# Kernel tuning notes

Hardware: AMD Instinct MI355X
Metric: run time of the kernel (lower is better)

## Reference

```python
import jax, jax.numpy as jnp
import numpy as np
import math

HEADS = 16
LN_EPS = 1e-5


def activation_quant(x):
    # 8-bit activation quant with straight-through estimator
    scale = 127.0 / jnp.clip(jnp.max(jnp.abs(x), axis=-1, keepdims=True), 1e-5)
    y = jnp.clip(jnp.round(x * scale), -128.0, 127.0) / scale
    return x + jax.lax.stop_gradient(y - x)


def weight_quant(w):
    # ternary {-1,0,1} weight quant with STE
    scale = 1.0 / jnp.clip(jnp.mean(jnp.abs(w)), 1e-5)
    wq = jnp.clip(jnp.round(w * scale), -1.0, 1.0) / scale
    return w + jax.lax.stop_gradient(wq - w)


def bitlinear(x, w):
    # F.layer_norm(x, x.shape[1:]) -> normalize jointly over (N, D), no affine
    mu = jnp.mean(x, axis=(1, 2), keepdims=True)
    var = jnp.var(x, axis=(1, 2), keepdims=True)
    xn = (x - mu) * jax.lax.rsqrt(var + LN_EPS)
    return activation_quant(xn) @ weight_quant(w).T


def setup_inputs() -> dict:
    key = jax.random.key(0)
    ks = jax.random.split(key, 6)
    B, N, D = 2, 2048, 1024
    x = jax.random.normal(ks[0], (B, N, D), dtype=jnp.float32)
    init = lambda k: jax.random.normal(k, (D, D), dtype=jnp.float32) * 0.02
    return {
        'x': x,
        'wq': init(ks[1]),
        'wk': init(ks[2]),
        'wv': init(ks[3]),
        'wg': init(ks[4]),
        'wo': init(ks[5]),
        'ln_w': jnp.ones((D,), dtype=jnp.float32),
        'ln_b': jnp.zeros((D,), dtype=jnp.float32),
    }


def reference(x, wq, wk, wv, wg, wo, ln_w, ln_b):
    B, N, D = x.shape
    H = HEADS
    hd = D // H
    scale = hd ** -0.5

    def split_heads(t):
        return t.reshape(B, N, H, hd).transpose(0, 2, 1, 3)  # [B,H,N,hd]

    q = split_heads(bitlinear(x, wq))
    k = split_heads(bitlinear(x, wk))
    v = split_heads(bitlinear(x, wv))

    attn = jnp.einsum('bhnd,bhmd->bhnm', q, k) * scale

    gammas = 1.0 - jnp.exp(jnp.linspace(math.log(1.0 / 32.0), math.log(1.0 / 512.0), H))
    idx = jnp.arange(N)
    dist = idx[:, None] - idx[None, :]                       # [N,N]
    decay = gammas[:, None, None] ** jnp.abs(dist)[None].astype(x.dtype)  # [H,N,N]
    causal = (dist >= 0).astype(x.dtype)[None]               # [1,N,N]
    scores = attn * (decay * causal)[None]                   # [B,H,N,N]

    y = jnp.einsum('bhnm,bhmd->bhnd', scores, v)
    y = y.transpose(0, 2, 1, 3).reshape(B, N, D)

    # LayerNorm over last dim with affine (torch nn.LayerNorm default)
    mu = jnp.mean(y, axis=-1, keepdims=True)
    var = jnp.var(y, axis=-1, keepdims=True)
    y = (y - mu) * jax.lax.rsqrt(var + LN_EPS) * ln_w + ln_b

    g = jax.nn.silu(bitlinear(x, wg))
    return bitlinear(y * g, wo)
```

## Files before the change

### kernel.cpp

```cpp
#include <hip/hip_runtime.h>
#include <math.h>

#define B_ 2
#define N_ 2048
#define D_ 1024
#define H_ 16
#define M_ (B_*N_)

typedef unsigned short u16;
typedef unsigned int u32;
typedef short bf16x8 __attribute__((ext_vector_type(8)));
typedef float f32x4 __attribute__((ext_vector_type(4)));

struct Ptr5 { const float* p[5]; };
struct GammaArg { float lg2[16]; };

static __device__ inline u16 f2bf(float f) {
  union { float f; unsigned u; } x; x.f = f;
  unsigned u = x.u;
  unsigned r = (u + 0x7fffu + ((u >> 16) & 1u)) >> 16;
  return (u16)r;
}
static __device__ inline float bf2f(u16 h) {
  union { unsigned u; float f; } x; x.u = ((unsigned)h) << 16; return x.f;
}
static __device__ inline bf16x8 ld8(const u16* p) {
  uint4 u = *(const uint4*)(p);
  return *reinterpret_cast<bf16x8*>(&u);
}
#define GLDS(g, l) __builtin_amdgcn_global_load_lds((const __attribute__((address_space(1))) u32*)(g), (__attribute__((address_space(3))) u32*)(l), 16, 0, 0)

__global__ void k_batch_stats_partial(const float* __restrict__ x, double* __restrict__ part) {
  int b = blockIdx.y, c = blockIdx.x, t = threadIdx.x;
  const float* p = x + (size_t)b*(N_*D_) + (size_t)c*32768;
  double s = 0.0, s2 = 0.0;
  for (int it = 0; it < 32; ++it) {
    float4 v = *(const float4*)(p + it*1024 + t*4);
    s  += (double)v.x + (double)v.y + (double)v.z + (double)v.w;
    s2 += (double)v.x*v.x + (double)v.y*v.y + (double)v.z*v.z + (double)v.w*v.w;
  }
  for (int o = 32; o > 0; o >>= 1) { s += __shfl_down(s,o); s2 += __shfl_down(s2,o); }
  __shared__ double lds[8];
  int w = t>>6, l = t&63;
  if (l==0) { lds[w*2]=s; lds[w*2+1]=s2; }
  __syncthreads();
  if (t==0) {
    part[(b*64+c)*2]   = lds[0]+lds[2]+lds[4]+lds[6];
    part[(b*64+c)*2+1] = lds[1]+lds[3]+lds[5]+lds[7];
  }
}

__global__ void k_batch_stats_final(const double* __restrict__ part, float* __restrict__ stats) {
  int b = blockIdx.x, t = threadIdx.x;
  double s = part[(b*64+t)*2], s2 = part[(b*64+t)*2+1];
  for (int o = 32; o > 0; o >>= 1) { s += __shfl_down(s,o); s2 += __shfl_down(s2,o); }
  if (t==0) {
    double inv = 1.0/(double)(N_*D_);
    double mu = s*inv, var = s2*inv - mu*mu;
    stats[b*2]   = (float)mu;
    stats[b*2+1] = rsqrtf((float)var + 1e-5f);
  }
}

__global__ void k_wmean_partial(Ptr5 W, double* __restrict__ part) {
  int wi = blockIdx.y, c = blockIdx.x, t = threadIdx.x;
  const float* p = W.p[wi] + (size_t)c*65536;
  double s = 0.0;
  for (int it = 0; it < 64; ++it) {
    float4 v = *(const float4*)(p + it*1024 + t*4);
    s += fabs((double)v.x)+fabs((double)v.y)+fabs((double)v.z)+fabs((double)v.w);
  }
  for (int o = 32; o > 0; o >>= 1) s += __shfl_down(s,o);
  __shared__ double lds[4];
  if ((t&63)==0) lds[t>>6]=s;
  __syncthreads();
  if (t==0) part[wi*16+c] = lds[0]+lds[1]+lds[2]+lds[3];
}

__global__ void k_wmean_final(const double* __restrict__ part, float* __restrict__ mw, float* __restrict__ invmw) {
  int wi = blockIdx.x, t = threadIdx.x;
  double s = (t<16) ? part[wi*16+t] : 0.0;
  for (int o = 8; o > 0; o >>= 1) s += __shfl_down(s,o);
  if (t==0) {
    double mean = s / (double)(D_*D_);
    float mwc = fmaxf((float)mean, 1e-5f);
    mw[wi] = mwc;
    invmw[wi] = 1.0f/mwc;
  }
}

__global__ void k_ternarize(Ptr5 W, const float* __restrict__ invmw, u16* __restrict__ wt) {
  int wi = blockIdx.y;
  float inv = invmw[wi];
  size_t off = (size_t)blockIdx.x*1024 + threadIdx.x*4;
  float4 v = *(const float4*)(W.p[wi] + off);
  ushort4 o4;
  o4.x = f2bf(fminf(fmaxf(rintf(v.x*inv),-1.f),1.f));
  o4.y = f2bf(fminf(fmaxf(rintf(v.y*inv),-1.f),1.f));
  o4.z = f2bf(fminf(fmaxf(rintf(v.z*inv),-1.f),1.f));
  o4.w = f2bf(fminf(fmaxf(rintf(v.w*inv),-1.f),1.f));
  *(ushort4*)(wt + (size_t)wi*(D_*D_) + off) = o4;
}

__global__ void k_quant_rows(const float* __restrict__ in, const float* __restrict__ stats,
                             u16* __restrict__ q, float* __restrict__ rowscale) {
  int m = blockIdx.x, t = threadIdx.x;
  int b = m >> 11;
  float mu = stats[b*2], rstd = stats[b*2+1];
  float4 v = *(const float4*)(in + (size_t)m*D_ + t*4);
  float xn0 = (v.x-mu)*rstd, xn1 = (v.y-mu)*rstd, xn2 = (v.z-mu)*rstd, xn3 = (v.w-mu)*rstd;
  float am = fmaxf(fmaxf(fabsf(xn0),fabsf(xn1)),fmaxf(fabsf(xn2),fabsf(xn3)));
  for (int o = 32; o > 0; o >>= 1) am = fmaxf(am, __shfl_xor(am,o));
  __shared__ float wm[4];
  int w = t>>6, l = t&63;
  if (l==0) wm[w]=am;
  __syncthreads();
  am = fmaxf(fmaxf(wm[0],wm[1]),fmaxf(wm[2],wm[3]));
  float clipped = fmaxf(am, 1e-5f);
  float sc = 127.0f/clipped;
  ushort4 o4;
  o4.x = f2bf(fminf(fmaxf(rintf(xn0*sc),-128.f),127.f));
  o4.y = f2bf(fminf(fmaxf(rintf(xn1*sc),-128.f),127.f));
  o4.z = f2bf(fminf(fmaxf(rintf(xn2*sc),-128.f),127.f));
  o4.w = f2bf(fminf(fmaxf(rintf(xn3*sc),-128.f),127.f));
  *(ushort4*)(q + (size_t)m*D_ + t*4) = o4;
  if (t==0) rowscale[m] = clipped/127.0f;
}

__global__ __launch_bounds__(256, 4) void k_gemm_qkvg(const u16* __restrict__ A, const u16* __restrict__ Wt,
                       const float* __restrict__ rowscale, const float* __restrict__ mw,
                       u16* __restrict__ qh, u16* __restrict__ kh, u16* __restrict__ vhT,
                       u16* __restrict__ gbufH) {
  __shared__ u16 smem[8192];
  int tid = threadIdx.x;
  int flat = blockIdx.y * gridDim.x + blockIdx.x;
  int swz = (flat & 7) * 128 + (flat >> 3);
  int mxi = swz & 31, nyi = swz >> 5;
  int m0 = mxi*128, n0g = nyi*128;
  int widx = nyi >> 3;
  int w = tid>>6, l = tid&63;
  int wm = (w>>1)*64, wn = (w&1)*64;
  int lr = l&15, lkg = l>>4;
  f32x4 acc[4][4];
  for (int i=0;i<4;++i) for (int j=0;j<4;++j) acc[i][j] = (f32x4){0.f,0.f,0.f,0.f};
  int c0 = tid, c1 = tid + 256;
  const u16* ga0 = A  + (size_t)(m0 + (c0>>2))*D_ + (c0&3)*8;
  const u16* ga1 = A  + (size_t)(m0 + (c1>>2))*D_ + (c1&3)*8;
  const u16* gb0 = Wt + (size_t)(n0g + (c0>>2))*D_ + (c0&3)*8;
  const u16* gb1 = Wt + (size_t)(n0g + (c1>>2))*D_ + (c1&3)*8;
  for (int k0 = 0; k0 < D_; k0 += 32) {
    __syncthreads();
    GLDS(ga0 + k0, &smem[w*512]);
    GLDS(ga1 + k0, &smem[2048 + w*512]);
    GLDS(gb0 + k0, &smem[4096 + w*512]);
    GLDS(gb1 + k0, &smem[6144 + w*512]);
    __syncthreads();
    bf16x8 a[4], b[4];
    #pragma unroll
    for (int i=0;i<4;++i) a[i] = ld8(&smem[(wm + i*16 + lr)*32 + lkg*8]);
    #pragma unroll
    for (int j=0;j<4;++j) b[j] = ld8(&smem[4096 + (wn + j*16 + lr)*32 + lkg*8]);
    #pragma unroll
    for (int i=0;i<4;++i)
      #pragma unroll
      for (int j=0;j<4;++j)
        acc[i][j] = __builtin_amdgcn_mfma_f32_16x16x32_bf16(a[i], b[j], acc[i][j], 0, 0, 0);
  }
  float sw = mw[widx];
  int bb0 = m0 >> 11;
  int h0 = (n0g >> 6) & 15;
  #pragma unroll
  for (int g = 0; g < 4; ++g) {
    __syncthreads();
    if (widx != 2) {
      if ((w>>1) == (g>>1)) {
        #pragma unroll
        for (int ii = 0; ii < 2; ++ii) {
          int i = (g&1)*2 + ii;
          #pragma unroll
          for (int j = 0; j < 4; ++j) {
            int col = wn + j*16 + lr;
            #pragma unroll
            for (int r = 0; r < 4; ++r) {
              int rloc = ii*16 + lkg*4 + r;
              int row = m0 + g*32 + rloc;
              float v = acc[i][j][r] * rowscale[row] * sw;
              if (widx == 3) v = v / (1.0f + __expf(-v));
              smem[rloc*136 + col] = f2bf(v);
            }
          }
        }
      }
    } else {
      if ((w&1) == (g>>1)) {
        #pragma unroll
        for (int jj = 0; jj < 2; ++jj) {
          int j = (g&1)*2 + jj;
          #pragma unroll
          for (int i = 0; i < 4; ++i) {
            #pragma unroll
            for (int r = 0; r < 4; ++r) {
              int rowrel = wm + i*16 + lkg*4 + r;
              float v = acc[i][j][r] * rowscale[m0 + rowrel] * sw;
              smem[(jj*16 + lr)*136 + rowrel] = f2bf(v);
            }
          }
        }
      }
    }
    __syncthreads();
    #pragma unroll
    for (int u = 0; u < 2; ++u) {
      int c = u*256 + tid;
      int rr = c >> 4, k8 = c & 15;
      uint4 val = *(const uint4*)&smem[rr*136 + k8*8];
      if (widx <= 1) {
        int row = m0 + g*32 + rr;
        int n = row & 2047;
        int h = h0 + (k8 >> 3);
        int e8 = (k8 & 7)*8;
        u16* dst = widx ? kh : qh;
        *(uint4*)&dst[(((size_t)((row>>11)*H_ + h))*N_ + n)*64 + e8] = val;
      } else if (widx == 2) {
        int ecol = n0g + g*32 + rr;
        int h = (ecol >> 6) & 15, e = ecol & 63;
        int n8 = (m0 & 2047) + k8*8;
        *(uint4*)&vhT[(((size_t)(bb0*H_ + h))*64 + e)*N_ + n8] = val;
      } else {
        int row = m0 + g*32 + rr;
        int d = (n0g & 1023) + k8*8;
        *(uint4*)&gbufH[(size_t)row*D_ + d] = val;
      }
    }
  }
}

__global__ __launch_bounds__(256) void k_state(const u16* __restrict__ kh, const u16* __restrict__ vhT,
                       float* __restrict__ Mbuf, GammaArg G) {
  __shared__ u16 kT[64][72];
  int c = blockIdx.x, bh = blockIdx.y;
  float lg = G.lg2[bh & 15];
  int tid = threadIdx.x, w = tid>>6, l = tid&63;
  int lr = l&15, lkg = l>>4;
  const size_t base = (size_t)bh * (N_*64);
  {
    int j = tid>>2, cs = (tid&3)*16;
    const u16* kp = kh + base + (size_t)(c*64 + j)*64 + cs;
    uint4 u0 = *(const uint4*)kp;
    uint4 u1 = *(const uint4*)(kp + 8);
    const u16* s0 = (const u16*)&u0;
    const u16* s1 = (const u16*)&u1;
    #pragma unroll
    for (int m2=0;m2<8;++m2) kT[cs+m2][j] = s0[m2];
    #pragma unroll
    for (int m2=0;m2<8;++m2) kT[cs+8+m2][j] = s1[m2];
  }
  __syncthreads();
  bf16x8 ah[2], al[2];
  #pragma unroll
  for (int kk=0;kk<2;++kk) {
    bf16x8 raw = ld8(vhT + base + (size_t)(w*16 + lr)*N_ + c*64 + kk*32 + lkg*8);
    #pragma unroll
    for (int m2=0;m2<8;++m2) {
      int j = kk*32 + lkg*8 + m2;
      float wj = exp2f((float)(64 - j) * lg);
      float p = bf2f((u16)raw[m2]) * wj;
      u16 hh = f2bf(p);
      ah[kk][m2] = (short)hh;
      al[kk][m2] = (short)f2bf(p - bf2f(hh));
    }
  }
  f32x4 macc[4];
  for (int t=0;t<4;++t) macc[t] = (f32x4){0.f,0.f,0.f,0.f};
  #pragma unroll
  for (int t=0;t<4;++t)
    #pragma unroll
    for (int kk=0;kk<2;++kk) {
      bf16x8 b = ld8(&kT[t*16 + lr][kk*32 + lkg*8]);
      macc[t] = __builtin_amdgcn_mfma_f32_16x16x32_bf16(ah[kk], b, macc[t], 0,0,0);
      macc[t] = __builtin_amdgcn_mfma_f32_16x16x32_bf16(al[kk], b, macc[t], 0,0,0);
    }
  float* mp = Mbuf + (size_t)(bh*32 + c)*4096;
  for (int t=0;t<4;++t) {
    #pragma unroll
    for (int r=0;r<4;++r)
      mp[(w*16 + lkg*4 + r)*64 + t*16 + lr] = macc[t][r];
  }
}

__global__ void k_scan(const float* __restrict__ Mbuf, u16* __restrict__ Shi, u16* __restrict__ Slo, GammaArg G) {
  int bx = blockIdx.x, bh = blockIdx.y;
  float g64 = exp2f(64.0f * G.lg2[bh & 15]);
  int e = bx*256 + threadIdx.x;
  size_t eb = (size_t)bh*32*4096 + e;
  float S = 0.0f;
  Shi[eb] = 0; Slo[eb] = 0;
  #pragma unroll
  for (int c = 1; c < 32; ++c) {
    S = g64*S + Mbuf[eb + (size_t)(c-1)*4096];
    u16 hh = f2bf(S);
    Shi[eb + (size_t)c*4096] = hh;
    Slo[eb + (size_t)c*4096] = f2bf(S - bf2f(hh));
  }
}

__global__ __launch_bounds__(256) void k_retB(const u16* __restrict__ qh, const u16* __restrict__ kh,
                       const u16* __restrict__ vhT, const u16* __restrict__ Shi, const u16* __restrict__ Slo,
                       float* __restrict__ y, GammaArg G) {
  __shared__ u16 pl[4][16][76];
  int c = blockIdx.x, bh = blockIdx.y;
  int b = bh >> 4, h = bh & 15;
  float lg = G.lg2[h];
  int tid = threadIdx.x, w = tid>>6, l = tid&63;
  int lr = l&15, lkg = l>>4;
  const size_t base = (size_t)bh * (N_*64);
  int nl_base = w*16 + lkg*4;
  bf16x8 qa[2];
  {
    const u16* qp = qh + base + (size_t)(c*64 + w*16 + lr)*64 + lkg*8;
    qa[0] = ld8(qp);
    qa[1] = ld8(qp + 32);
  }
  f32x4 yc[4];
  for (int t=0;t<4;++t) yc[t] = (f32x4){0.f,0.f,0.f,0.f};
  {
    const u16* sp = Shi + (size_t)(bh*32 + c)*4096;
    const u16* sq = Slo + (size_t)(bh*32 + c)*4096;
    #pragma unroll
    for (int kk=0;kk<2;++kk)
      #pragma unroll
      for (int t=0;t<4;++t) {
        int off = (t*16 + lr)*64 + kk*32 + lkg*8;
        yc[t] = __builtin_amdgcn_mfma_f32_16x16x32_bf16(qa[kk], ld8(sp + off), yc[t], 0,0,0);
        yc[t] = __builtin_amdgcn_mfma_f32_16x16x32_bf16(qa[kk], ld8(sq + off), yc[t], 0,0,0);
      }
  }
  f32x4 sacc[4];
  for (int jt=0;jt<4;++jt) sacc[jt] = (f32x4){0.f,0.f,0.f,0.f};
  #pragma unroll
  for (int jt=0;jt<4;++jt) {
    const u16* kp = kh + base + (size_t)(c*64 + jt*16 + lr)*64 + lkg*8;
    sacc[jt] = __builtin_amdgcn_mfma_f32_16x16x32_bf16(qa[0], ld8(kp),    sacc[jt], 0,0,0);
    sacc[jt] = __builtin_amdgcn_mfma_f32_16x16x32_bf16(qa[1], ld8(kp+32), sacc[jt], 0,0,0);
  }
  #pragma unroll
  for (int jt=0;jt<4;++jt)
    #pragma unroll
    for (int r=0;r<4;++r) {
      int d = (nl_base + r) - (jt*16 + lr);
      float p = (d >= 0) ? sacc[jt][r]*0.125f*exp2f((float)d*lg) : 0.0f;
      pl[w][lkg*4+r][jt*16+lr] = f2bf(p);
    }
  f32x4 yacc[4];
  for (int t=0;t<4;++t) yacc[t] = (f32x4){0.f,0.f,0.f,0.f};
  #pragma unroll
  for (int kk2=0;kk2<2;++kk2) {
    bf16x8 pa = *(bf16x8*)&pl[w][lr][kk2*32 + lkg*8];
    #pragma unroll
    for (int t=0;t<4;++t) {
      bf16x8 vb = ld8(vhT + base + (size_t)(t*16 + lr)*N_ + c*64 + kk2*32 + lkg*8);
      yacc[t] = __builtin_amdgcn_mfma_f32_16x16x32_bf16(pa, vb, yacc[t], 0,0,0);
    }
  }
  float cw[4];
  #pragma unroll
  for (int r=0;r<4;++r) cw[r] = 0.125f * exp2f((float)(nl_base + r) * lg);
  for (int t=0;t<4;++t) {
    #pragma unroll
    for (int r=0;r<4;++r) {
      int n = c*64 + nl_base + r;
      int col = h*64 + t*16 + lr;
      y[((size_t)(b*N_ + n))*D_ + col] = yacc[t][r] + cw[r]*yc[t][r];
    }
  }
}

__global__ __launch_bounds__(256, 4) void k_gemm(const u16* __restrict__ A, const u16* __restrict__ Bt,
                       const float* __restrict__ rowscale, const float* __restrict__ mw, int widx,
                       float* __restrict__ outF) {
  __shared__ u16 As[128*32];
  __shared__ u16 Bs[64*32];
  int tid = threadIdx.x;
  int flat = blockIdx.y * gridDim.x + blockIdx.x;
  int swz = (flat & 7) * 64 + (flat >> 3);
  int m0 = (swz & 31)*128, n0 = (swz >> 5)*64;
  int w = tid>>6, l = tid&63;
  int wm = (w>>1)*64, wn = (w&1)*32;
  int lr = l&15, lkg = l>>4;
  f32x4 acc[4][2];
  for (int i=0;i<4;++i) for (int j=0;j<2;++j) acc[i][j] = (f32x4){0.f,0.f,0.f,0.f};
  int c0 = tid, c1 = tid + 256;
  const u16* ga0 = A  + (size_t)(m0 + (c0>>2))*D_ + (c0&3)*8;
  const u16* ga1 = A  + (size_t)(m0 + (c1>>2))*D_ + (c1&3)*8;
  const u16* gb0 = Bt + (size_t)(n0 + (c0>>2))*D_ + (c0&3)*8;
  for (int k0 = 0; k0 < D_; k0 += 32) {
    __syncthreads();
    GLDS(ga0 + k0, &As[w*512]);
    GLDS(ga1 + k0, &As[2048 + w*512]);
    GLDS(gb0 + k0, &Bs[w*512]);
    __syncthreads();
    bf16x8 a[4], b[2];
    for (int i=0;i<4;++i) a[i] = ld8(&As[(wm + i*16 + lr)*32 + lkg*8]);
    for (int j=0;j<2;++j) b[j] = ld8(&Bs[(wn + j*16 + lr)*32 + lkg*8]);
    for (int i=0;i<4;++i)
      for (int j=0;j<2;++j)
        acc[i][j] = __builtin_amdgcn_mfma_f32_16x16x32_bf16(a[i], b[j], acc[i][j], 0, 0, 0);
  }
  float sw = mw[widx];
  for (int i=0;i<4;++i) {
    int rowb = m0 + wm + i*16 + lkg*4;
    for (int j=0;j<2;++j) {
      int col = n0 + wn + j*16 + lr;
      #pragma unroll
      for (int r=0;r<4;++r)
        outF[(size_t)(rowb+r)*D_ + col] = acc[i][j][r] * rowscale[rowb+r] * sw;
    }
  }
}

__global__ void k_ln_mul(const float* __restrict__ y, const u16* __restrict__ gH,
                         const float* __restrict__ lnw, const float* __restrict__ lnb,
                         float* __restrict__ z, double* __restrict__ zrow) {
  int m = blockIdx.x, t = threadIdx.x;
  float4 v = *(const float4*)(y + (size_t)m*D_ + t*4);
  double s  = (double)v.x + (double)v.y + (double)v.z + (double)v.w;
  double s2 = (double)v.x*v.x + (double)v.y*v.y + (double)v.z*v.z + (double)v.w*v.w;
  __shared__ double lds[8];
  int w = t>>6, l = t&63;
  for (int o = 32; o > 0; o >>= 1) { s += __shfl_down(s,o); s2 += __shfl_down(s2,o); }
  if (l==0) { lds[w*2]=s; lds[w*2+1]=s2; }
  __syncthreads();
  double ts = lds[0]+lds[2]+lds[4]+lds[6], ts2 = lds[1]+lds[3]+lds[5]+lds[7];
  float mu = (float)(ts/(double)D_);
  float var = (float)(ts2/(double)D_) - mu*mu;
  float rstd = rsqrtf(var + 1e-5f);
  ushort4 gv4 = *(const ushort4*)(gH + (size_t)m*D_ + t*4);
  float g0 = bf2f(gv4.x), g1 = bf2f(gv4.y), g2 = bf2f(gv4.z), g3 = bf2f(gv4.w);
  float4 lw = *(const float4*)(lnw + t*4);
  float4 lb = *(const float4*)(lnb + t*4);
  float z0 = ((v.x-mu)*rstd*lw.x + lb.x)*g0;
  float z1 = ((v.y-mu)*rstd*lw.y + lb.y)*g1;
  float z2 = ((v.z-mu)*rstd*lw.z + lb.z)*g2;
  float z3 = ((v.w-mu)*rstd*lw.w + lb.w)*g3;
  float4 zo; zo.x=z0; zo.y=z1; zo.z=z2; zo.w=z3;
  *(float4*)(z + (size_t)m*D_ + t*4) = zo;
  double zs  = (double)z0 + (double)z1 + (double)z2 + (double)z3;
  double zs2 = (double)z0*z0 + (double)z1*z1 + (double)z2*z2 + (double)z3*z3;
  for (int o = 32; o > 0; o >>= 1) { zs += __shfl_down(zs,o); zs2 += __shfl_down(zs2,o); }
  __syncthreads();
  if (l==0) { lds[w*2]=zs; lds[w*2+1]=zs2; }
  __syncthreads();
  if (t==0) {
    zrow[m*2]   = lds[0]+lds[2]+lds[4]+lds[6];
    zrow[m*2+1] = lds[1]+lds[3]+lds[5]+lds[7];
  }
}

__global__ void k_zstats_final(const double* __restrict__ zrow, float* __restrict__ stats) {
  int b = blockIdx.x, t = threadIdx.x;
  double s=0.0, s2=0.0;
  for (int k=0;k<8;++k) {
    int m = b*2048 + k*256 + t;
    s += zrow[m*2]; s2 += zrow[m*2+1];
  }
  for (int o = 32; o > 0; o >>= 1) { s += __shfl_down(s,o); s2 += __shfl_down(s2,o); }
  __shared__ double lds[8];
  int w = t>>6, l = t&63;
  if (l==0) { lds[w*2]=s; lds[w*2+1]=s2; }
  __syncthreads();
  if (t==0) {
    double ts = lds[0]+lds[2]+lds[4]+lds[6], ts2 = lds[1]+lds[3]+lds[5]+lds[7];
    double inv = 1.0/(double)(N_*D_);
    double mu = ts*inv, var = ts2*inv - mu*mu;
    stats[b*2]   = (float)mu;
    stats[b*2+1] = rsqrtf((float)var + 1e-5f);
  }
}

extern "C" void kernel_launch(void* const* d_in, const int* in_sizes, int n_in,
                              void* d_out, int out_size, void* d_ws, size_t ws_size,
                              hipStream_t stream) {
  const float* x = (const float*)d_in[0];
  Ptr5 W;
  for (int i = 0; i < 5; ++i) W.p[i] = (const float*)d_in[1+i];
  const float* lnw = (const float*)d_in[6];
  const float* lnb = (const float*)d_in[7];

  char* ws = (char*)d_ws;
  float*  xstats = (float*)(ws + 0);
  float*  zstats = (float*)(ws + 64);
  float*  mw     = (float*)(ws + 128);
  float*  invmw  = (float*)(ws + 192);
  double* part1  = (double*)(ws + 256);
  double* wpart  = (double*)(ws + 2304);
  float*  inv1   = (float*)(ws + 3072);
  float*  inv2   = (float*)(ws + 19456);
  double* zrow   = (double*)(ws + 35840);
  u16*    wt     = (u16*)(ws + 101376);
  u16*    qx     = (u16*)(ws + 10587136);
  u16*    qh     = (u16*)(ws + 18975744);
  u16*    kh     = (u16*)(ws + 27364352);
  u16*    vhT    = (u16*)(ws + 35752960);
  u16*    gbufH  = (u16*)(ws + 44141568);
  float*  ybuf   = (float*)(ws + 60918784);
  float*  zbuf   = (float*)(ws + 77696000);
  float*  Mbuf   = (float*)(ws + 77696000);
  u16*    Shi    = (u16*)(ws + 10587136);
  u16*    Slo    = (u16*)(ws + 101376);
  u16*    qz     = qx;

  GammaArg G;
  {
    double l0 = log(1.0/32.0), l1 = log(1.0/512.0);
    for (int h = 0; h < 16; ++h) {
      float t = (float)(l0 + (l1-l0)*((double)h/15.0));
      float gm = 1.0f - expf(t);
      G.lg2[h] = (float)log2((double)gm);
    }
  }

  dim3 b256(256);
  hipLaunchKernelGGL(k_batch_stats_partial, dim3(64, B_), b256, 0, stream, x, part1);
  hipLaunchKernelGGL(k_batch_stats_final, dim3(B_), dim3(64), 0, stream, part1, xstats);
  hipLaunchKernelGGL(k_wmean_partial, dim3(16, 5), b256, 0, stream, W, wpart);
  hipLaunchKernelGGL(k_wmean_final, dim3(5), dim3(64), 0, stream, wpart, mw, invmw);
  hipLaunchKernelGGL(k_ternarize, dim3(1024, 5), b256, 0, stream, W, invmw, wt);
  hipLaunchKernelGGL(k_quant_rows, dim3(M_), b256, 0, stream, x, xstats, qx, inv1);

  hipLaunchKernelGGL(k_gemm_qkvg, dim3(32, 32), b256, 0, stream, qx, wt, inv1, mw, qh, kh, vhT, gbufH);

  hipLaunchKernelGGL(k_state, dim3(32, 32), b256, 0, stream, kh, vhT, Mbuf, G);
  hipLaunchKernelGGL(k_scan, dim3(16, 32), b256, 0, stream, Mbuf, Shi, Slo, G);
  hipLaunchKernelGGL(k_retB, dim3(32, 32), b256, 0, stream, qh, kh, vhT, Shi, Slo, ybuf, G);

  hipLaunchKernelGGL(k_ln_mul, dim3(M_), b256, 0, stream, ybuf, gbufH, lnw, lnb, zbuf, zrow);
  hipLaunchKernelGGL(k_zstats_final, dim3(B_), b256, 0, stream, zrow, zstats);
  hipLaunchKernelGGL(k_quant_rows, dim3(M_), b256, 0, stream, zbuf, zstats, qz, inv2);
  hipLaunchKernelGGL(k_gemm, dim3(32,16), b256, 0, stream, qz, wt + (size_t)4*1048576, inv2, mw, 4, (float*)d_out);
}
```

Before: 238.4 us.

## Merge prologue stat/quant kernels and use 64-wide K tiles with XOR-swizzled LDS

```diff
diff --git a/kernel.cpp b/kernel.cpp
--- a/kernel.cpp
+++ b/kernel.cpp
@@ -30,76 +30,110 @@
 }
 #define GLDS(g, l) __builtin_amdgcn_global_load_lds((const __attribute__((address_space(1))) u32*)(g), (__attribute__((address_space(3))) u32*)(l), 16, 0, 0)
 
-__global__ void k_batch_stats_partial(const float* __restrict__ x, double* __restrict__ part) {
-  int b = blockIdx.y, c = blockIdx.x, t = threadIdx.x;
-  const float* p = x + (size_t)b*(N_*D_) + (size_t)c*32768;
-  double s = 0.0, s2 = 0.0;
-  for (int it = 0; it < 32; ++it) {
-    float4 v = *(const float4*)(p + it*1024 + t*4);
-    s  += (double)v.x + (double)v.y + (double)v.z + (double)v.w;
-    s2 += (double)v.x*v.x + (double)v.y*v.y + (double)v.z*v.z + (double)v.w*v.w;
-  }
-  for (int o = 32; o > 0; o >>= 1) { s += __shfl_down(s,o); s2 += __shfl_down(s2,o); }
+__global__ void k_stats_all(const float* __restrict__ x, Ptr5 W,
+                            double* __restrict__ part1, double* __restrict__ wpart) {
+  int bx = blockIdx.x, t = threadIdx.x;
+  int w = t>>6, l = t&63;
   __shared__ double lds[8];
+  if (bx < 128) {
+    int b = bx >> 6, c = bx & 63;
+    const float* p = x + (size_t)b*(N_*D_) + (size_t)c*32768;
+    double s = 0.0, s2 = 0.0;
+    for (int it = 0; it < 32; ++it) {
+      float4 v = *(const float4*)(p + it*1024 + t*4);
+      s  += (double)v.x + (double)v.y + (double)v.z + (double)v.w;
+      s2 += (double)v.x*v.x + (double)v.y*v.y + (double)v.z*v.z + (double)v.w*v.w;
+    }
+    for (int o = 32; o > 0; o >>= 1) { s += __shfl_down(s,o); s2 += __shfl_down(s2,o); }
+    if (l==0) { lds[w*2]=s; lds[w*2+1]=s2; }
+    __syncthreads();
+    if (t==0) {
+      part1[(b*64+c)*2]   = lds[0]+lds[2]+lds[4]+lds[6];
+      part1[(b*64+c)*2+1] = lds[1]+lds[3]+lds[5]+lds[7];
+    }
+  } else {
+    int i = bx - 128;
+    int wi = i >> 4, c = i & 15;
+    const float* p = W.p[wi] + (size_t)c*65536;
+    double s = 0.0;
+    for (int it = 0; it < 64; ++it) {
+      float4 v = *(const float4*)(p + it*1024 + t*4);
+      s += fabs((double)v.x)+fabs((double)v.y)+fabs((double)v.z)+fabs((double)v.w);
+    }
+    for (int o = 32; o > 0; o >>= 1) s += __shfl_down(s,o);
+    if (l==0) lds[w]=s;
+    __syncthreads();
+    if (t==0) wpart[wi*16+c] = lds[0]+lds[1]+lds[2]+lds[3];
+  }
+}
+
+__global__ void k_finals(const double* __restrict__ part1, const double* __restrict__ wpart,
+                         float* __restrict__ xstats, float* __restrict__ mw, float* __restrict__ invmw) {
+  int t = threadIdx.x;
   int w = t>>6, l = t&63;
-  if (l==0) { lds[w*2]=s; lds[w*2+1]=s2; }
-  __syncthreads();
-  if (t==0) {
-    part[(b*64+c)*2]   = lds[0]+lds[2]+lds[4]+lds[6];
-    part[(b*64+c)*2+1] = lds[1]+lds[3]+lds[5]+lds[7];
-  }
-}
-
-__global__ void k_batch_stats_final(const double* __restrict__ part, float* __restrict__ stats) {
-  int b = blockIdx.x, t = threadIdx.x;
-  double s = part[(b*64+t)*2], s2 = part[(b*64+t)*2+1];
-  for (int o = 32; o > 0; o >>= 1) { s += __shfl_down(s,o); s2 += __shfl_down(s2,o); }
-  if (t==0) {
-    double inv = 1.0/(double)(N_*D_);
-    double mu = s*inv, var = s2*inv - mu*mu;
-    stats[b*2]   = (float)mu;
-    stats[b*2+1] = rsqrtf((float)var + 1e-5f);
-  }
-}
-
-__global__ void k_wmean_partial(Ptr5 W, double* __restrict__ part) {
-  int wi = blockIdx.y, c = blockIdx.x, t = threadIdx.x;
-  const float* p = W.p[wi] + (size_t)c*65536;
-  double s = 0.0;
-  for (int it = 0; it < 64; ++it) {
-    float4 v = *(const float4*)(p + it*1024 + t*4);
-    s += fabs((double)v.x)+fabs((double)v.y)+fabs((double)v.z)+fabs((double)v.w);
-  }
-  for (int o = 32; o > 0; o >>= 1) s += __shfl_down(s,o);
-  __shared__ double lds[4];
-  if ((t&63)==0) lds[t>>6]=s;
-  __syncthreads();
-  if (t==0) part[wi*16+c] = lds[0]+lds[1]+lds[2]+lds[3];
-}
-
-__global__ void k_wmean_final(const double* __restrict__ part, float* __restrict__ mw, float* __restrict__ invmw) {
-  int wi = blockIdx.x, t = threadIdx.x;
-  double s = (t<16) ? part[wi*16+t] : 0.0;
-  for (int o = 8; o > 0; o >>= 1) s += __shfl_down(s,o);
-  if (t==0) {
-    double mean = s / (double)(D_*D_);
-    float mwc = fmaxf((float)mean, 1e-5f);
-    mw[wi] = mwc;
-    invmw[wi] = 1.0f/mwc;
-  }
-}
-
-__global__ void k_ternarize(Ptr5 W, const float* __restrict__ invmw, u16* __restrict__ wt) {
-  int wi = blockIdx.y;
-  float inv = invmw[wi];
-  size_t off = (size_t)blockIdx.x*1024 + threadIdx.x*4;
-  float4 v = *(const float4*)(W.p[wi] + off);
-  ushort4 o4;
-  o4.x = f2bf(fminf(fmaxf(rintf(v.x*inv),-1.f),1.f));
-  o4.y = f2bf(fminf(fmaxf(rintf(v.y*inv),-1.f),1.f));
-  o4.z = f2bf(fminf(fmaxf(rintf(v.z*inv),-1.f),1.f));
-  o4.w = f2bf(fminf(fmaxf(rintf(v.w*inv),-1.f),1.f));
-  *(ushort4*)(wt + (size_t)wi*(D_*D_) + off) = o4;
+  if (w < 2) {
+    double s = part1[(w*64+l)*2], s2 = part1[(w*64+l)*2+1];
+    for (int o = 32; o > 0; o >>= 1) { s += __shfl_down(s,o); s2 += __shfl_down(s2,o); }
+    if (l==0) {
+      double inv = 1.0/(double)(N_*D_);
+      double mu = s*inv, var = s2*inv - mu*mu;
+      xstats[w*2]   = (float)mu;
+      xstats[w*2+1] = rsqrtf((float)var + 1e-5f);
+    }
+  } else {
+    int idx = (w-2)*4 + (l>>4);
+    int j = l&15;
+    if (idx < 5) {
+      double s = wpart[idx*16+j];
+      for (int o = 8; o > 0; o >>= 1) s += __shfl_down(s,o);
+      if (j==0) {
+        double mean = s / (double)(D_*D_);
+        float mwc = fmaxf((float)mean, 1e-5f);
+        mw[idx] = mwc;
+        invmw[idx] = 1.0f/mwc;
+      }
+    }
+  }
+}
+
+__global__ void k_ternquant(Ptr5 W, const float* __restrict__ invmw, u16* __restrict__ wt,
+                            const float* __restrict__ x, const float* __restrict__ xstats,
+                            u16* __restrict__ qx, float* __restrict__ inv1) {
+  int bx = blockIdx.x, t = threadIdx.x;
+  if (bx < 5120) {
+    int wi = bx >> 10;
+    float inv = invmw[wi];
+    size_t off = (size_t)(bx & 1023)*1024 + t*4;
+    float4 v = *(const float4*)(W.p[wi] + off);
+    ushort4 o4;
+    o4.x = f2bf(fminf(fmaxf(rintf(v.x*inv),-1.f),1.f));
+    o4.y = f2bf(fminf(fmaxf(rintf(v.y*inv),-1.f),1.f));
+    o4.z = f2bf(fminf(fmaxf(rintf(v.z*inv),-1.f),1.f));
+    o4.w = f2bf(fminf(fmaxf(rintf(v.w*inv),-1.f),1.f));
+    *(ushort4*)(wt + (size_t)wi*(D_*D_) + off) = o4;
+  } else {
+    int m = bx - 5120;
+    int b = m >> 11;
+    float mu = xstats[b*2], rstd = xstats[b*2+1];
+    float4 v = *(const float4*)(x + (size_t)m*D_ + t*4);
+    float xn0 = (v.x-mu)*rstd, xn1 = (v.y-mu)*rstd, xn2 = (v.z-mu)*rstd, xn3 = (v.w-mu)*rstd;
+    float am = fmaxf(fmaxf(fabsf(xn0),fabsf(xn1)),fmaxf(fabsf(xn2),fabsf(xn3)));
+    for (int o = 32; o > 0; o >>= 1) am = fmaxf(am, __shfl_xor(am,o));
+    __shared__ float wm[4];
+    int w = t>>6, l = t&63;
+    if (l==0) wm[w]=am;
+    __syncthreads();
+    am = fmaxf(fmaxf(wm[0],wm[1]),fmaxf(wm[2],wm[3]));
+    float clipped = fmaxf(am, 1e-5f);
+    float sc = 127.0f/clipped;
+    ushort4 o4;
+    o4.x = f2bf(fminf(fmaxf(rintf(xn0*sc),-128.f),127.f));
+    o4.y = f2bf(fminf(fmaxf(rintf(xn1*sc),-128.f),127.f));
+    o4.z = f2bf(fminf(fmaxf(rintf(xn2*sc),-128.f),127.f));
+    o4.w = f2bf(fminf(fmaxf(rintf(xn3*sc),-128.f),127.f));
+    *(ushort4*)(qx + (size_t)m*D_ + t*4) = o4;
+    if (t==0) inv1[m] = clipped/127.0f;
+  }
 }
 
 __global__ void k_quant_rows(const float* __restrict__ in, const float* __restrict__ stats,
@@ -131,7 +165,7 @@
                        const float* __restrict__ rowscale, const float* __restrict__ mw,
                        u16* __restrict__ qh, u16* __restrict__ kh, u16* __restrict__ vhT,
                        u16* __restrict__ gbufH) {
-  __shared__ u16 smem[8192];
+  __shared__ u16 smem[16384];
   int tid = threadIdx.x;
   int flat = blockIdx.y * gridDim.x + blockIdx.x;
   int swz = (flat & 7) * 128 + (flat >> 3);
@@ -143,28 +177,42 @@
   int lr = l&15, lkg = l>>4;
   f32x4 acc[4][4];
   for (int i=0;i<4;++i) for (int j=0;j<4;++j) acc[i][j] = (f32x4){0.f,0.f,0.f,0.f};
-  int c0 = tid, c1 = tid + 256;
-  const u16* ga0 = A  + (size_t)(m0 + (c0>>2))*D_ + (c0&3)*8;
-  const u16* ga1 = A  + (size_t)(m0 + (c1>>2))*D_ + (c1&3)*8;
-  const u16* gb0 = Wt + (size_t)(n0g + (c0>>2))*D_ + (c0&3)*8;
-  const u16* gb1 = Wt + (size_t)(n0g + (c1>>2))*D_ + (c1&3)*8;
-  for (int k0 = 0; k0 < D_; k0 += 32) {
-    __syncthreads();
-    GLDS(ga0 + k0, &smem[w*512]);
-    GLDS(ga1 + k0, &smem[2048 + w*512]);
-    GLDS(gb0 + k0, &smem[4096 + w*512]);
-    GLDS(gb1 + k0, &smem[6144 + w*512]);
-    __syncthreads();
-    bf16x8 a[4], b[4];
-    #pragma unroll
-    for (int i=0;i<4;++i) a[i] = ld8(&smem[(wm + i*16 + lr)*32 + lkg*8]);
-    #pragma unroll
-    for (int j=0;j<4;++j) b[j] = ld8(&smem[4096 + (wn + j*16 + lr)*32 + lkg*8]);
-    #pragma unroll
-    for (int i=0;i<4;++i)
-      #pragma unroll
-      for (int j=0;j<4;++j)
-        acc[i][j] = __builtin_amdgcn_mfma_f32_16x16x32_bf16(a[i], b[j], acc[i][j], 0, 0, 0);
+  const u16* gaS[4]; const u16* gbS[4];
+  #pragma unroll
+  for (int i=0;i<4;++i) {
+    int c = i*256 + tid;
+    int row = c>>3, sslot = (c&7) ^ (row&7);
+    gaS[i] = A  + (size_t)(m0 + row)*D_ + sslot*8;
+    gbS[i] = Wt + (size_t)(n0g + row)*D_ + sslot*8;
+  }
+  for (int k0 = 0; k0 < D_; k0 += 64) {
+    __syncthreads();
+    #pragma unroll
+    for (int i=0;i<4;++i) {
+      GLDS(gaS[i] + k0, &smem[i*2048 + w*512]);
+      GLDS(gbS[i] + k0, &smem[8192 + i*2048 + w*512]);
+    }
+    __syncthreads();
+    #pragma unroll
+    for (int kk=0;kk<2;++kk) {
+      int s = kk*4 + lkg;
+      bf16x8 a[4], b[4];
+      #pragma unroll
+      for (int i=0;i<4;++i) {
+        int r = wm + i*16 + lr;
+        a[i] = ld8(&smem[r*64 + (s ^ (r&7))*8]);
+      }
+      #pragma unroll
+      for (int j=0;j<4;++j) {
+        int r = wn + j*16 + lr;
+        b[j] = ld8(&smem[8192 + r*64 + (s ^ (r&7))*8]);
+      }
+      #pragma unroll
+      for (int i=0;i<4;++i)
+        #pragma unroll
+        for (int j=0;j<4;++j)
+          acc[i][j] = __builtin_amdgcn_mfma_f32_16x16x32_bf16(a[i], b[j], acc[i][j], 0, 0, 0);
+    }
   }
   float sw = mw[widx];
   int bb0 = m0 >> 11;
@@ -378,8 +426,8 @@
 __global__ __launch_bounds__(256, 4) void k_gemm(const u16* __restrict__ A, const u16* __restrict__ Bt,
                        const float* __restrict__ rowscale, const float* __restrict__ mw, int widx,
                        float* __restrict__ outF) {
-  __shared__ u16 As[128*32];
-  __shared__ u16 Bs[64*32];
+  __shared__ u16 As[8192];
+  __shared__ u16 Bs[4096];
   int tid = threadIdx.x;
   int flat = blockIdx.y * gridDim.x + blockIdx.x;
   int swz = (flat & 7) * 64 + (flat >> 3);
@@ -389,22 +437,41 @@
   int lr = l&15, lkg = l>>4;
   f32x4 acc[4][2];
   for (int i=0;i<4;++i) for (int j=0;j<2;++j) acc[i][j] = (f32x4){0.f,0.f,0.f,0.f};
-  int c0 = tid, c1 = tid + 256;
-  const u16* ga0 = A  + (size_t)(m0 + (c0>>2))*D_ + (c0&3)*8;
-  const u16* ga1 = A  + (size_t)(m0 + (c1>>2))*D_ + (c1&3)*8;
-  const u16* gb0 = Bt + (size_t)(n0 + (c0>>2))*D_ + (c0&3)*8;
-  for (int k0 = 0; k0 < D_; k0 += 32) {
-    __syncthreads();
-    GLDS(ga0 + k0, &As[w*512]);
-    GLDS(ga1 + k0, &As[2048 + w*512]);
-    GLDS(gb0 + k0, &Bs[w*512]);
-    __syncthreads();
-    bf16x8 a[4], b[2];
-    for (int i=0;i<4;++i) a[i] = ld8(&As[(wm + i*16 + lr)*32 + lkg*8]);
-    for (int j=0;j<2;++j) b[j] = ld8(&Bs[(wn + j*16 + lr)*32 + lkg*8]);
-    for (int i=0;i<4;++i)
-      for (int j=0;j<2;++j)
-        acc[i][j] = __builtin_amdgcn_mfma_f32_16x16x32_bf16(a[i], b[j], acc[i][j], 0, 0, 0);
+  const u16* gaS[4]; const u16* gbS[2];
+  #pragma unroll
+  for (int i=0;i<4;++i) {
+    int c = i*256 + tid;
+    int row = c>>3, sslot = (c&7) ^ (row&7);
+    gaS[i] = A + (size_t)(m0 + row)*D_ + sslot*8;
+    if (i < 2) gbS[i] = Bt + (size_t)(n0 + row)*D_ + sslot*8;
+  }
+  for (int k0 = 0; k0 < D_; k0 += 64) {
+    __syncthreads();
+    #pragma unroll
+    for (int i=0;i<4;++i) GLDS(gaS[i] + k0, &As[i*2048 + w*512]);
+    #pragma unroll
+    for (int i=0;i<2;++i) GLDS(gbS[i] + k0, &Bs[i*2048 + w*512]);
+    __syncthreads();
+    #pragma unroll
+    for (int kk=0;kk<2;++kk) {
+      int s = kk*4 + lkg;
+      bf16x8 a[4], b[2];
+      #pragma unroll
+      for (int i=0;i<4;++i) {
+        int r = wm + i*16 + lr;
+        a[i] = ld8(&As[r*64 + (s ^ (r&7))*8]);
+      }
+      #pragma unroll
+      for (int j=0;j<2;++j) {
+        int r = wn + j*16 + lr;
+        b[j] = ld8(&Bs[r*64 + (s ^ (r&7))*8]);
+      }
+      #pragma unroll
+      for (int i=0;i<4;++i)
+        #pragma unroll
+        for (int j=0;j<2;++j)
+          acc[i][j] = __builtin_amdgcn_mfma_f32_16x16x32_bf16(a[i], b[j], acc[i][j], 0, 0, 0);
+    }
   }
   float sw = mw[widx];
   for (int i=0;i<4;++i) {
@@ -520,12 +587,9 @@
   }
 
   dim3 b256(256);
-  hipLaunchKernelGGL(k_batch_stats_partial, dim3(64, B_), b256, 0, stream, x, part1);
-  hipLaunchKernelGGL(k_batch_stats_final, dim3(B_), dim3(64), 0, stream, part1, xstats);
-  hipLaunchKernelGGL(k_wmean_partial, dim3(16, 5), b256, 0, stream, W, wpart);
-  hipLaunchKernelGGL(k_wmean_final, dim3(5), dim3(64), 0, stream, wpart, mw, invmw);
-  hipLaunchKernelGGL(k_ternarize, dim3(1024, 5), b256, 0, stream, W, invmw, wt);
-  hipLaunchKernelGGL(k_quant_rows, dim3(M_), b256, 0, stream, x, xstats, qx, inv1);
+  hipLaunchKernelGGL(k_stats_all, dim3(208), b256, 0, stream, x, W, part1, wpart);
+  hipLaunchKernelGGL(k_finals, dim3(1), b256, 0, stream, part1, wpart, xstats, mw, invmw);
+  hipLaunchKernelGGL(k_ternquant, dim3(9216), b256, 0, stream, W, invmw, wt, x, xstats, qx, inv1);
 
   hipLaunchKernelGGL(k_gemm_qkvg, dim3(32, 32), b256, 0, stream, qx, wt, inv1, mw, qh, kh, vhT, gbufH);
 
```

New measurement: 236.7 us. Within noise of the previous version (-0.7%).
